# Performance work log

Measured on AMD Instinct MI355X. Metric: run time of the kernel, lower is better.

The kernel has to match this reference:

```python
import jax, jax.numpy as jnp
import numpy as np

T = 16          # timesteps
BATCH = 8       # video clips -> leading dim of x is BATCH*T = 128
C_IN = 768      # fixed by nn.Conv2d(768, redu_dim, 1)
D = 256         # redu_dim
K = 64          # num_centers
H = W = 28
EPS = 1e-12     # torch F.normalize eps


def _conv(x, w, padding):
    # x: [N,C,H,W], w: [O,I,kh,kw]
    return jax.lax.conv_general_dilated(
        x, w, window_strides=(1, 1), padding=padding,
        dimension_numbers=('NCHW', 'OIHW', 'NCHW'))


def setup_inputs() -> dict:
    key = jax.random.key(0)
    ks = jax.random.split(key, 9)
    x = jax.random.normal(ks[0], (BATCH * T, C_IN, H, W), dtype=jnp.float32)
    redu_w = jax.random.normal(ks[1], (D, C_IN, 1, 1), jnp.float32) * 0.02
    redu_b = jnp.zeros((D,), jnp.float32)
    share_w = jax.random.normal(ks[2], (K, D, 1, 1), jnp.float32) * 0.05
    share_b = jnp.zeros((K,), jnp.float32)
    U_z = jax.random.normal(ks[3], (K, K, 3, 3), jnp.float32) * 0.04
    U_r = jax.random.normal(ks[4], (K, K, 3, 3), jnp.float32) * 0.04
    U_h = jax.random.normal(ks[5], (K, K, 3, 3), jnp.float32) * 0.04
    centers = jax.random.normal(ks[6], (K, D), jnp.float32) * 0.06
    return {"x": x, "redu_w": redu_w, "redu_b": redu_b,
            "share_w": share_w, "share_b": share_b,
            "U_z": U_z, "U_r": U_r, "U_h": U_h,
            "centers": centers, "timesteps": T}


def reference(x, redu_w, redu_b, share_w, share_b, U_z, U_r, U_h, centers, timesteps):
    t = timesteps
    bt, _, h, w = x.shape
    b = bt // t
    k = share_w.shape[0]
    d = redu_w.shape[0]

    # channel reduction (1x1 conv)
    xr = _conv(x, redu_w, 'VALID') + redu_b[None, :, None, None]        # [bt,d,h,w]
    # shared assignment logits (1x1 conv)
    wxb = _conv(xr, share_w, 'VALID') + share_b[None, :, None, None]     # [bt,k,h,w]
    wxb = wxb.reshape(b, t, k, h, w).transpose(1, 0, 2, 3, 4)            # [t,b,k,h,w]

    # sequential ConvGRU over timesteps
    h0 = jnp.zeros((b, k, h, w), x.dtype)
    def step(h_tm1, w_t):
        z = jax.nn.sigmoid(w_t + _conv(h_tm1, U_z, 'SAME'))
        r = jax.nn.sigmoid(w_t + _conv(h_tm1, U_r, 'SAME'))
        hh = jnp.tanh(w_t + _conv(r * h_tm1, U_h, 'SAME'))
        h_new = (1.0 - z) * hh + z * h_tm1
        return h_new, h_new
    _, hs = jax.lax.scan(step, h0, wxb)                                  # [t,b,k,h,w]

    assign = hs.transpose(1, 0, 2, 3, 4).reshape(b * t, k, h * w)        # [bt,k,hw]
    # softmax over centers per spatial location
    assign = jax.nn.softmax(assign, axis=1)

    # VLAD aggregation
    a_sum = assign.sum(axis=-1, keepdims=True)                           # [bt,k,1]
    a = a_sum * centers[None]                                            # [bt,k,d]
    xf = xr.reshape(b * t, d, h * w)                                     # [bt,d,hw]
    vlad = jnp.einsum('bkp,bdp->bkd', assign, xf) - a                    # [bt,k,d]

    vlad = vlad.reshape(b, t, k, d).sum(axis=1)                          # [b,k,d]
    # intra-norm over feature dim, then global L2 norm
    vlad = vlad / jnp.maximum(jnp.linalg.norm(vlad, axis=2, keepdims=True), EPS)
    vlad = vlad.reshape(b, k * d)
    vlad = vlad / jnp.maximum(jnp.linalg.norm(vlad, axis=1, keepdims=True), EPS)
    return vlad
```

## Files before the change

kernel.cpp:

```cpp
#include <hip/hip_runtime.h>
#include <hip/hip_bf16.h>

#define T_ 16
#define B_ 8
#define CIN 768
#define D_ 256
#define K_ 64
#define HW 784
#define W_ 28

typedef short short8 __attribute__((ext_vector_type(8)));
typedef short short4v __attribute__((ext_vector_type(4)));
typedef float floatx4 __attribute__((ext_vector_type(4)));
typedef unsigned short ushort_t;

__device__ __forceinline__ unsigned short f2bf(float x) {
    union { float f; unsigned u; } v; v.f = x;
    unsigned u = v.u;
    unsigned r = (u + 0x7fffu + ((u >> 16) & 1u)) >> 16;
    return (unsigned short)r;
}
__device__ __forceinline__ float bf2f(unsigned short h) {
    union { unsigned u; float f; } v; v.u = ((unsigned)h) << 16; return v.f;
}

__device__ __forceinline__ float block_reduce_sum_256(float v) {
    for (int off = 32; off > 0; off >>= 1) v += __shfl_down(v, off, 64);
    __shared__ float red[4];
    __shared__ float tot;
    int lane = threadIdx.x & 63, wid = threadIdx.x >> 6;
    if (lane == 0) red[wid] = v;
    __syncthreads();
    if (threadIdx.x == 0) tot = red[0] + red[1] + red[2] + red[3];
    __syncthreads();
    return tot;
}

__global__ __launch_bounds__(256) void cvt_weights(
    const float* __restrict__ rw, const float* __restrict__ sw,
    const float* __restrict__ Uz, const float* __restrict__ Ur,
    const float* __restrict__ Uh,
    ushort_t* __restrict__ whi, ushort_t* __restrict__ wlo,
    ushort_t* __restrict__ shi, ushort_t* __restrict__ slo,
    ushort_t* __restrict__ azh, ushort_t* __restrict__ azl,
    ushort_t* __restrict__ ahh, ushort_t* __restrict__ ahl)
{
    int i = blockIdx.x * 256 + threadIdx.x;
    const int nR = D_ * CIN;
    const int nS = K_ * D_;
    const int nZR = 128 * 576;
    const int nH = 64 * 576;
    if (i < nR) {
        float x = rw[i];
        unsigned short h = f2bf(x);
        whi[i] = h; wlo[i] = f2bf(x - bf2f(h));
    } else if (i < nR + nS) {
        int j = i - nR;
        float x = sw[j];
        unsigned short h = f2bf(x);
        shi[j] = h; slo[j] = f2bf(x - bf2f(h));
    } else if (i < nR + nS + nZR) {
        int j = i - nR - nS;
        int row = j / 576, kk = j - row * 576;
        int tap = kk >> 6, c = kk & 63;
        const float* U = (row < 64) ? Uz : Ur;
        float x = U[(((size_t)(row & 63)) * 64 + c) * 9 + tap];
        unsigned short h = f2bf(x);
        azh[j] = h; azl[j] = f2bf(x - bf2f(h));
    } else if (i < nR + nS + nZR + nH) {
        int j = i - nR - nS - nZR;
        int row = j / 576, kk = j - row * 576;
        int tap = kk >> 6, c = kk & 63;
        float x = Uh[(((size_t)row) * 64 + c) * 9 + tap];
        unsigned short h = f2bf(x);
        ahh[j] = h; ahl[j] = f2bf(x - bf2f(h));
    }
}

template<int BM>
__global__ __launch_bounds__(256, 2) void mfma_conv1x1(
    const float* __restrict__ X, const ushort_t* __restrict__ Whi,
    const ushort_t* __restrict__ Wlo, const float* __restrict__ bias,
    float* __restrict__ Out, int Kdim)
{
    const int nt = blockIdx.x, bt = blockIdx.z;
    const int p0 = nt * 112;
    const int tid = threadIdx.x, lane = tid & 63, wv = tid >> 6;
    const float* Xb = X + (size_t)bt * Kdim * HW;
    float* Ob = Out + (size_t)bt * BM * HW;

    __shared__ ushort_t lA[2][BM * 40];
    __shared__ ushort_t lB[2][112 * 40];

    constexpr int NI = (BM == 256) ? 7 : 2;
    floatx4 acc[4][NI];
#pragma unroll
    for (int a = 0; a < 4; ++a)
#pragma unroll
        for (int b = 0; b < NI; ++b) acc[a][b] = (floatx4){0.f, 0.f, 0.f, 0.f};

    const int NKS = Kdim / 32;
    for (int ks = 0; ks < NKS; ++ks) {
        const int k0 = ks * 32;
#pragma unroll
        for (int i = 0; i < BM / 64; ++i) {
            int ch = tid + i * 256;
            int m = ch >> 2, j = ch & 3;
            uint4 hv = *(const uint4*)(Whi + (size_t)m * Kdim + k0 + j * 8);
            uint4 lv = *(const uint4*)(Wlo + (size_t)m * Kdim + k0 + j * 8);
            *(uint4*)&lA[0][m * 40 + j * 8] = hv;
            *(uint4*)&lA[1][m * 40 + j * 8] = lv;
        }
#pragma unroll
        for (int i = 0; i < 14; ++i) {
            int e = tid + i * 256;
            int cc = e / 112, pp = e - cc * 112;
            float xv = Xb[(size_t)(k0 + cc) * HW + p0 + pp];
            unsigned short h = f2bf(xv);
            lB[0][pp * 40 + cc] = h;
            lB[1][pp * 40 + cc] = f2bf(xv - bf2f(h));
        }
        __syncthreads();

        short8 ahi[4], alo[4];
        const int mbase = (BM == 256) ? wv * 64 : 0;
        const int koff = (lane >> 4) * 8;
#pragma unroll
        for (int mi = 0; mi < 4; ++mi) {
            int m = mbase + mi * 16 + (lane & 15);
            ahi[mi] = *(const short8*)&lA[0][m * 40 + koff];
            alo[mi] = *(const short8*)&lA[1][m * 40 + koff];
        }
        if constexpr (BM == 256) {
#pragma unroll
            for (int ni = 0; ni < 7; ++ni) {
                int n = ni * 16 + (lane & 15);
                short8 bhi = *(const short8*)&lB[0][n * 40 + koff];
                short8 blo = *(const short8*)&lB[1][n * 40 + koff];
#pragma unroll
                for (int mi = 0; mi < 4; ++mi) {
                    acc[mi][ni] = __builtin_amdgcn_mfma_f32_16x16x32_bf16(ahi[mi], bhi, acc[mi][ni], 0, 0, 0);
                    acc[mi][ni] = __builtin_amdgcn_mfma_f32_16x16x32_bf16(ahi[mi], blo, acc[mi][ni], 0, 0, 0);
                    acc[mi][ni] = __builtin_amdgcn_mfma_f32_16x16x32_bf16(alo[mi], bhi, acc[mi][ni], 0, 0, 0);
                }
            }
        } else {
#pragma unroll
            for (int nj = 0; nj < 2; ++nj) {
                int ni = wv * 2 + nj;
                if (ni >= 7) break;
                int n = ni * 16 + (lane & 15);
                short8 bhi = *(const short8*)&lB[0][n * 40 + koff];
                short8 blo = *(const short8*)&lB[1][n * 40 + koff];
#pragma unroll
                for (int mi = 0; mi < 4; ++mi) {
                    acc[mi][nj] = __builtin_amdgcn_mfma_f32_16x16x32_bf16(ahi[mi], bhi, acc[mi][nj], 0, 0, 0);
                    acc[mi][nj] = __builtin_amdgcn_mfma_f32_16x16x32_bf16(ahi[mi], blo, acc[mi][nj], 0, 0, 0);
                    acc[mi][nj] = __builtin_amdgcn_mfma_f32_16x16x32_bf16(alo[mi], bhi, acc[mi][nj], 0, 0, 0);
                }
            }
        }
        __syncthreads();
    }

    if constexpr (BM == 256) {
#pragma unroll
        for (int mi = 0; mi < 4; ++mi) {
            int m0g = wv * 64 + mi * 16 + ((lane >> 4) << 2);
#pragma unroll
            for (int ni = 0; ni < 7; ++ni) {
                int p = p0 + ni * 16 + (lane & 15);
#pragma unroll
                for (int r = 0; r < 4; ++r)
                    Ob[(size_t)(m0g + r) * HW + p] = acc[mi][ni][r] + bias[m0g + r];
            }
        }
    } else {
#pragma unroll
        for (int nj = 0; nj < 2; ++nj) {
            int ni = wv * 2 + nj;
            if (ni >= 7) break;
            int p = p0 + ni * 16 + (lane & 15);
#pragma unroll
            for (int mi = 0; mi < 4; ++mi) {
                int m0g = mi * 16 + ((lane >> 4) << 2);
#pragma unroll
                for (int r = 0; r < 4; ++r)
                    Ob[(size_t)(m0g + r) * HW + p] = acc[mi][nj][r] + bias[m0g + r];
            }
        }
    }
}

__device__ __forceinline__ void stage_tile(
    const ushort_t* __restrict__ ghi, const ushort_t* __restrict__ glo,
    ushort_t* Bhi, ushort_t* Blo, int y0, int tid)
{
    for (int e = tid; e < 6 * 30 * 8; e += 256) {
        int r = e / 240, rem = e - r * 240;
        int lx = rem >> 3, j = rem & 7;
        int gy = y0 - 1 + r, gx = lx - 1;
        short8 vh = {0, 0, 0, 0, 0, 0, 0, 0};
        short8 vl = {0, 0, 0, 0, 0, 0, 0, 0};
        if (gy >= 0 && gy < 28 && gx >= 0 && gx < 28) {
            size_t go = ((size_t)(gy * 28 + gx)) * 64 + j * 8;
            vh = *(const short8*)(ghi + go);
            vl = *(const short8*)(glo + go);
        }
        int lo = (r * 30 + lx) * 72 + j * 8;
        *(short8*)&Bhi[lo] = vh;
        *(short8*)&Blo[lo] = vl;
    }
}

__device__ __forceinline__ void gru_gemm(
    const ushort_t* __restrict__ Ahi, const ushort_t* __restrict__ Alo,
    int arow, int Astride,
    const ushort_t* Bhi, const ushort_t* Blo, int lane, floatx4 acc[7])
{
    const int koff8 = (lane >> 4) * 8;
    const int li = lane & 15;
    int yb[7], xb[7];
#pragma unroll
    for (int nf = 0; nf < 7; ++nf) {
        int pp = nf * 16 + li;
        yb[nf] = pp / 28; xb[nf] = pp - yb[nf] * 28;
    }
    for (int tap = 0; tap < 9; ++tap) {
        int dy = tap / 3, dx = tap - dy * 3;
#pragma unroll
        for (int ch = 0; ch < 2; ++ch) {
            int kk = tap * 64 + ch * 32 + koff8;
            short8 ahi = *(const short8*)(Ahi + (size_t)arow * Astride + kk);
            short8 alo = *(const short8*)(Alo + (size_t)arow * Astride + kk);
            int cbase = ch * 32 + koff8;
#pragma unroll
            for (int nf = 0; nf < 7; ++nf) {
                int o = ((yb[nf] + dy) * 30 + xb[nf] + dx) * 72 + cbase;
                short8 bhi = *(const short8*)&Bhi[o];
                short8 blo = *(const short8*)&Blo[o];
                acc[nf] = __builtin_amdgcn_mfma_f32_16x16x32_bf16(ahi, bhi, acc[nf], 0, 0, 0);
                acc[nf] = __builtin_amdgcn_mfma_f32_16x16x32_bf16(ahi, blo, acc[nf], 0, 0, 0);
                acc[nf] = __builtin_amdgcn_mfma_f32_16x16x32_bf16(alo, bhi, acc[nf], 0, 0, 0);
            }
        }
    }
}

__global__ __launch_bounds__(256, 2) void gru_zr_mfma(
    const ushort_t* __restrict__ hhi, const ushort_t* __restrict__ hlo,
    const ushort_t* __restrict__ azh, const ushort_t* __restrict__ azl,
    const float* __restrict__ wxb, const float* __restrict__ hprev_f,
    float* __restrict__ zbuf, ushort_t* __restrict__ rhi, ushort_t* __restrict__ rlo,
    int t)
{
    int rt = blockIdx.x, b = blockIdx.y, half = blockIdx.z;
    int y0 = rt * 4;
    int tid = threadIdx.x, lane = tid & 63, wv = tid >> 6;

    __shared__ ushort_t Bhi[6 * 30 * 72];
    __shared__ ushort_t Blo[6 * 30 * 72];
    stage_tile(hhi + (size_t)b * HW * 64, hlo + (size_t)b * HW * 64, Bhi, Blo, y0, tid);
    __syncthreads();

    floatx4 acc[7];
#pragma unroll
    for (int nf = 0; nf < 7; ++nf) acc[nf] = (floatx4){0.f, 0.f, 0.f, 0.f};

    int arow = half * 64 + wv * 16 + (lane & 15);
    gru_gemm(azh, azl, arow, 576, Bhi, Blo, lane, acc);

    int kbase = wv * 16 + ((lane >> 4) << 2);
    const float* wx = wxb + (((size_t)b * T_ + t) * K_) * HW;
    const float* hp = hprev_f + (size_t)b * K_ * HW;
#pragma unroll
    for (int nf = 0; nf < 7; ++nf) {
        int p = y0 * 28 + nf * 16 + (lane & 15);
        if (half == 0) {
#pragma unroll
            for (int r = 0; r < 4; ++r) {
                int k = kbase + r;
                float g = 1.f / (1.f + __expf(-(wx[(size_t)k * HW + p] + acc[nf][r])));
                zbuf[((size_t)b * K_ + k) * HW + p] = g;
            }
        } else {
            short4v vh, vl;
#pragma unroll
            for (int r = 0; r < 4; ++r) {
                int k = kbase + r;
                float g = 1.f / (1.f + __expf(-(wx[(size_t)k * HW + p] + acc[nf][r])));
                float rh = g * hp[(size_t)k * HW + p];
                unsigned short h = f2bf(rh);
                vh[r] = h; vl[r] = f2bf(rh - bf2f(h));
            }
            size_t o = (size_t)(b * HW + p) * 64 + kbase;
            *(short4v*)(rhi + o) = vh;
            *(short4v*)(rlo + o) = vl;
        }
    }
}

__global__ __launch_bounds__(256, 2) void gru_h_mfma(
    const ushort_t* __restrict__ rhi, const ushort_t* __restrict__ rlo,
    const ushort_t* __restrict__ ahh, const ushort_t* __restrict__ ahl,
    const float* __restrict__ wxb, const float* __restrict__ hprev_f,
    const float* __restrict__ zbuf, float* __restrict__ hs_t,
    ushort_t* __restrict__ hhi, ushort_t* __restrict__ hlo, int t)
{
    int rt = blockIdx.x, b = blockIdx.y;
    int y0 = rt * 4;
    int tid = threadIdx.x, lane = tid & 63, wv = tid >> 6;

    __shared__ ushort_t Bhi[6 * 30 * 72];
    __shared__ ushort_t Blo[6 * 30 * 72];
    stage_tile(rhi + (size_t)b * HW * 64, rlo + (size_t)b * HW * 64, Bhi, Blo, y0, tid);
    __syncthreads();

    floatx4 acc[7];
#pragma unroll
    for (int nf = 0; nf < 7; ++nf) acc[nf] = (floatx4){0.f, 0.f, 0.f, 0.f};

    int arow = wv * 16 + (lane & 15);
    gru_gemm(ahh, ahl, arow, 576, Bhi, Blo, lane, acc);

    int kbase = wv * 16 + ((lane >> 4) << 2);
    const float* wx = wxb + (((size_t)b * T_ + t) * K_) * HW;
    const float* hp = hprev_f + (size_t)b * K_ * HW;
#pragma unroll
    for (int nf = 0; nf < 7; ++nf) {
        int p = y0 * 28 + nf * 16 + (lane & 15);
        short4v vh, vl;
#pragma unroll
        for (int r = 0; r < 4; ++r) {
            int k = kbase + r;
            float xv = wx[(size_t)k * HW + p] + acc[nf][r];
            float e2 = __expf(2.f * xv);
            float th = 1.f - 2.f / (e2 + 1.f);
            float z = zbuf[((size_t)b * K_ + k) * HW + p];
            float hpv = hp[(size_t)k * HW + p];
            float hn = (1.f - z) * th + z * hpv;
            hs_t[((size_t)b * K_ + k) * HW + p] = hn;
            unsigned short h = f2bf(hn);
            vh[r] = h; vl[r] = f2bf(hn - bf2f(h));
        }
        size_t o = (size_t)(b * HW + p) * 64 + kbase;
        *(short4v*)(hhi + o) = vh;
        *(short4v*)(hlo + o) = vl;
    }
}

__global__ __launch_bounds__(256) void softmax_k(float* __restrict__ hs)
{
    int q = blockIdx.x;
    float* base = hs + (size_t)q * K_ * HW;
    for (int p = threadIdx.x; p < HW; p += 256) {
        float v[64];
        float m = -1e30f;
#pragma unroll
        for (int k = 0; k < 64; ++k) {
            v[k] = base[(size_t)k * HW + p];
            m = fmaxf(m, v[k]);
        }
        float s = 0.f;
#pragma unroll
        for (int k = 0; k < 64; ++k) {
            v[k] = __expf(v[k] - m);
            s += v[k];
        }
        float inv = 1.f / s;
#pragma unroll
        for (int k = 0; k < 64; ++k)
            base[(size_t)k * HW + p] = v[k] * inv;
    }
}

__global__ __launch_bounds__(256) void asum_k(const float* __restrict__ hs,
                                              float* __restrict__ asum)
{
    int bid = blockIdx.x; int b = bid >> 6, k = bid & 63;
    float s = 0.f;
    for (int t = 0; t < T_; ++t) {
        const float* row = hs + (((size_t)t * B_ + b) * K_ + k) * HW;
        for (int p = threadIdx.x; p < HW; p += 256) s += row[p];
    }
    float tot = block_reduce_sum_256(s);
    if (threadIdx.x == 0) asum[bid] = tot;
}

__global__ __launch_bounds__(256) void vlad_k(const float* __restrict__ assign,
    const float* __restrict__ xr, float* __restrict__ vladt)
{
    int dt = blockIdx.x, t = blockIdx.y, b = blockIdx.z;
    int q = t * B_ + b, bt = b * T_ + t, d0 = dt * 64;
    const float* ab = assign + (size_t)q * K_ * HW;
    const float* xb = xr + (size_t)bt * D_ * HW;
    __shared__ float As[16][68];
    __shared__ float Xs[16][68];
    int tx = threadIdx.x & 15, ty = threadIdx.x >> 4;
    float acc[4][4] = {{0.f}};

    for (int p0 = 0; p0 < HW; p0 += 16) {
#pragma unroll
        for (int it = 0; it < 4; ++it) {
            int e = threadIdx.x + it * 256;
            int row = e >> 4, pp = e & 15;
            As[pp][row] = ab[(size_t)row * HW + p0 + pp];
            Xs[pp][row] = xb[(size_t)(d0 + row) * HW + p0 + pp];
        }
        __syncthreads();
#pragma unroll
        for (int pp = 0; pp < 16; ++pp) {
            float4 a = *(const float4*)&As[pp][ty * 4];
            float4 xv = *(const float4*)&Xs[pp][tx * 4];
            float av[4] = {a.x, a.y, a.z, a.w};
            float xvv[4] = {xv.x, xv.y, xv.z, xv.w};
#pragma unroll
            for (int r = 0; r < 4; ++r)
#pragma unroll
                for (int s = 0; s < 4; ++s)
                    acc[r][s] = fmaf(av[r], xvv[s], acc[r][s]);
        }
        __syncthreads();
    }
#pragma unroll
    for (int r = 0; r < 4; ++r) {
        int k = ty * 4 + r;
        float4 o = {acc[r][0], acc[r][1], acc[r][2], acc[r][3]};
        *(float4*)&vladt[((size_t)bt * K_ + k) * D_ + d0 + tx * 4] = o;
    }
}

__global__ __launch_bounds__(256) void norm1_k(const float* __restrict__ vladt,
    const float* __restrict__ asum, const float* __restrict__ centers,
    float* __restrict__ out)
{
    int bid = blockIdx.x; int b = bid >> 6, k = bid & 63; int d = threadIdx.x;
    float acc = 0.f;
#pragma unroll
    for (int t = 0; t < T_; ++t)
        acc += vladt[(((size_t)b * T_ + t) * K_ + k) * D_ + d];
    acc -= asum[bid] * centers[(size_t)k * D_ + d];
    float ss = block_reduce_sum_256(acc * acc);
    float n = fmaxf(sqrtf(ss), 1e-12f);
    out[((size_t)b * K_ + k) * D_ + d] = acc / n;
}

__global__ __launch_bounds__(256) void norm2_k(float* __restrict__ out)
{
    int b = blockIdx.x;
    float* v = out + (size_t)b * (K_ * D_);
    float s = 0.f;
    for (int i = threadIdx.x; i < K_ * D_; i += 256) {
        float x = v[i];
        s = fmaf(x, x, s);
    }
    float tot = block_reduce_sum_256(s);
    float n = fmaxf(sqrtf(tot), 1e-12f);
    for (int i = threadIdx.x; i < K_ * D_; i += 256) v[i] = v[i] / n;
}

extern "C" void kernel_launch(void* const* d_in, const int* in_sizes, int n_in,
                              void* d_out, int out_size, void* d_ws, size_t ws_size,
                              hipStream_t stream)
{
    const float* x       = (const float*)d_in[0];
    const float* redu_w  = (const float*)d_in[1];
    const float* redu_b  = (const float*)d_in[2];
    const float* share_w = (const float*)d_in[3];
    const float* share_b = (const float*)d_in[4];
    const float* Uz      = (const float*)d_in[5];
    const float* Ur      = (const float*)d_in[6];
    const float* Uh      = (const float*)d_in[7];
    const float* centers = (const float*)d_in[8];

    float* ws = (float*)d_ws;
    const size_t SZ_XR   = (size_t)128 * D_ * HW;
    const size_t SZ_WXB  = (size_t)128 * K_ * HW;
    const size_t SZ_HS   = (size_t)T_ * B_ * K_ * HW;
    const size_t SZ_PLANE= (size_t)B_ * K_ * HW;

    float* xr    = ws;
    float* wxb   = xr + SZ_XR;
    float* hs    = wxb + SZ_WXB;
    float* h0    = hs + SZ_HS;
    float* zbuf  = h0 + SZ_PLANE;
    float* asumb = zbuf + SZ_PLANE;
    float* wsplit= asumb + 512;
    float* area  = wsplit + 323584;

    ushort_t* whi = (ushort_t*)wsplit;
    ushort_t* wlo = whi + 196608;
    ushort_t* shi = wlo + 196608;
    ushort_t* slo = shi + 16384;
    ushort_t* azh = slo + 16384;
    ushort_t* azl = azh + 73728;
    ushort_t* ahh = azl + 73728;
    ushort_t* ahl = ahh + 36864;

    float* vladt = area;
    ushort_t* hhi = (ushort_t*)area;
    ushort_t* hlo = hhi + SZ_PLANE;
    ushort_t* rhi = hlo + SZ_PLANE;
    ushort_t* rlo = rhi + SZ_PLANE;

    hipMemsetAsync(h0, 0, SZ_PLANE * sizeof(float), stream);
    hipMemsetAsync(hhi, 0, 2 * SZ_PLANE * sizeof(ushort_t), stream);

    cvt_weights<<<dim3((D_ * CIN + K_ * D_ + 128 * 576 + 64 * 576 + 255) / 256),
                  256, 0, stream>>>(redu_w, share_w, Uz, Ur, Uh,
                                    whi, wlo, shi, slo, azh, azl, ahh, ahl);

    mfma_conv1x1<256><<<dim3(7, 1, 128), 256, 0, stream>>>(x, whi, wlo, redu_b, xr, CIN);
    mfma_conv1x1<64><<<dim3(7, 1, 128), 256, 0, stream>>>(xr, shi, slo, share_b, wxb, D_);

    for (int t = 0; t < T_; ++t) {
        const float* hp = (t == 0) ? h0 : hs + (size_t)(t - 1) * SZ_PLANE;
        gru_zr_mfma<<<dim3(7, 8, 2), 256, 0, stream>>>(hhi, hlo, azh, azl, wxb, hp,
                                                       zbuf, rhi, rlo, t);
        gru_h_mfma<<<dim3(7, 8), 256, 0, stream>>>(rhi, rlo, ahh, ahl, wxb, hp, zbuf,
                                                   hs + (size_t)t * SZ_PLANE, hhi, hlo, t);
    }

    softmax_k<<<128, 256, 0, stream>>>(hs);
    asum_k<<<512, 256, 0, stream>>>(hs, asumb);

    vlad_k<<<dim3(4, 16, 8), 256, 0, stream>>>(hs, xr, vladt);
    norm1_k<<<512, 256, 0, stream>>>(vladt, asumb, centers, (float*)d_out);
    norm2_k<<<8, 256, 0, stream>>>((float*)d_out);
}
```

Before: 795.5 us.

## Split GRU conv tiles to one row per block and stream conv1x1 weights from global

The GRU z/r and h kernels now process one image row per block instead of four, launching four times as many blocks (224/448 instead of 56/112) with a smaller 3-row LDS halo and two MFMA fragments per wave. This spreads the small sequential per-timestep launches across more CUs. It also re-reads the halo rows more often and wastes four lanes in the second fragment. The 1x1 conv kernels drop the LDS staging of weights, loading A fragments directly from global, and vectorise the X staging into 8-channel short8 writes. They also raise launch-bound occupancy hints.

```diff
diff --git a/kernel.cpp b/kernel.cpp
--- a/kernel.cpp
+++ b/kernel.cpp
@@ -77,8 +77,8 @@
     }
 }
 
-template<int BM>
-__global__ __launch_bounds__(256, 2) void mfma_conv1x1(
+template<int BM, int MINW>
+__global__ __launch_bounds__(256, MINW) void mfma_conv1x1(
     const float* __restrict__ X, const ushort_t* __restrict__ Whi,
     const ushort_t* __restrict__ Wlo, const float* __restrict__ bias,
     float* __restrict__ Out, int Kdim)
@@ -89,7 +89,6 @@
     const float* Xb = X + (size_t)bt * Kdim * HW;
     float* Ob = Out + (size_t)bt * BM * HW;
 
-    __shared__ ushort_t lA[2][BM * 40];
     __shared__ ushort_t lB[2][112 * 40];
 
     constexpr int NI = (BM == 256) ? 7 : 2;
@@ -98,38 +97,36 @@
     for (int a = 0; a < 4; ++a)
 #pragma unroll
         for (int b = 0; b < NI; ++b) acc[a][b] = (floatx4){0.f, 0.f, 0.f, 0.f};
+
+    const int koff = (lane >> 4) * 8;
+    const int mbase = (BM == 256) ? wv * 64 : 0;
 
     const int NKS = Kdim / 32;
     for (int ks = 0; ks < NKS; ++ks) {
         const int k0 = ks * 32;
 #pragma unroll
-        for (int i = 0; i < BM / 64; ++i) {
-            int ch = tid + i * 256;
-            int m = ch >> 2, j = ch & 3;
-            uint4 hv = *(const uint4*)(Whi + (size_t)m * Kdim + k0 + j * 8);
-            uint4 lv = *(const uint4*)(Wlo + (size_t)m * Kdim + k0 + j * 8);
-            *(uint4*)&lA[0][m * 40 + j * 8] = hv;
-            *(uint4*)&lA[1][m * 40 + j * 8] = lv;
-        }
-#pragma unroll
-        for (int i = 0; i < 14; ++i) {
-            int e = tid + i * 256;
-            int cc = e / 112, pp = e - cc * 112;
-            float xv = Xb[(size_t)(k0 + cc) * HW + p0 + pp];
-            unsigned short h = f2bf(xv);
-            lB[0][pp * 40 + cc] = h;
-            lB[1][pp * 40 + cc] = f2bf(xv - bf2f(h));
+        for (int u = tid; u < 448; u += 256) {
+            int j = u / 112, pp = u - j * 112;
+            const float* xp = Xb + (size_t)(k0 + j * 8) * HW + p0 + pp;
+            short8 vh, vl;
+#pragma unroll
+            for (int c = 0; c < 8; ++c) {
+                float xv = xp[(size_t)c * HW];
+                unsigned short h = f2bf(xv);
+                vh[c] = (short)h;
+                vl[c] = (short)f2bf(xv - bf2f(h));
+            }
+            *(short8*)&lB[0][pp * 40 + j * 8] = vh;
+            *(short8*)&lB[1][pp * 40 + j * 8] = vl;
         }
         __syncthreads();
 
         short8 ahi[4], alo[4];
-        const int mbase = (BM == 256) ? wv * 64 : 0;
-        const int koff = (lane >> 4) * 8;
 #pragma unroll
         for (int mi = 0; mi < 4; ++mi) {
             int m = mbase + mi * 16 + (lane & 15);
-            ahi[mi] = *(const short8*)&lA[0][m * 40 + koff];
-            alo[mi] = *(const short8*)&lA[1][m * 40 + koff];
+            ahi[mi] = *(const short8*)(Whi + (size_t)m * Kdim + k0 + koff);
+            alo[mi] = *(const short8*)(Wlo + (size_t)m * Kdim + k0 + koff);
         }
         if constexpr (BM == 256) {
 #pragma unroll
@@ -192,11 +189,11 @@
     }
 }
 
-__device__ __forceinline__ void stage_tile(
+__device__ __forceinline__ void stage_tile3(
     const ushort_t* __restrict__ ghi, const ushort_t* __restrict__ glo,
     ushort_t* Bhi, ushort_t* Blo, int y0, int tid)
 {
-    for (int e = tid; e < 6 * 30 * 8; e += 256) {
+    for (int e = tid; e < 3 * 30 * 8; e += 256) {
         int r = e / 240, rem = e - r * 240;
         int lx = rem >> 3, j = rem & 7;
         int gy = y0 - 1 + r, gx = lx - 1;
@@ -213,69 +210,70 @@
     }
 }
 
-__device__ __forceinline__ void gru_gemm(
-    const ushort_t* __restrict__ Ahi, const ushort_t* __restrict__ Alo,
-    int arow, int Astride,
-    const ushort_t* Bhi, const ushort_t* Blo, int lane, floatx4 acc[7])
+__device__ __forceinline__ void gru_gemm1(
+    const ushort_t* __restrict__ Ahi, const ushort_t* __restrict__ Alo, int arow,
+    const ushort_t* Bhi, const ushort_t* Blo, int lane, floatx4 acc[2])
 {
     const int koff8 = (lane >> 4) * 8;
     const int li = lane & 15;
-    int yb[7], xb[7];
-#pragma unroll
-    for (int nf = 0; nf < 7; ++nf) {
-        int pp = nf * 16 + li;
-        yb[nf] = pp / 28; xb[nf] = pp - yb[nf] * 28;
-    }
+    const int xb0 = li;
+    const int xb1 = (li < 12) ? 16 + li : 0;
+#pragma unroll
     for (int tap = 0; tap < 9; ++tap) {
-        int dy = tap / 3, dx = tap - dy * 3;
+        const int dy = tap / 3, dx = tap - dy * 3;
 #pragma unroll
         for (int ch = 0; ch < 2; ++ch) {
             int kk = tap * 64 + ch * 32 + koff8;
-            short8 ahi = *(const short8*)(Ahi + (size_t)arow * Astride + kk);
-            short8 alo = *(const short8*)(Alo + (size_t)arow * Astride + kk);
+            short8 ahi = *(const short8*)(Ahi + (size_t)arow * 576 + kk);
+            short8 alo = *(const short8*)(Alo + (size_t)arow * 576 + kk);
             int cbase = ch * 32 + koff8;
-#pragma unroll
-            for (int nf = 0; nf < 7; ++nf) {
-                int o = ((yb[nf] + dy) * 30 + xb[nf] + dx) * 72 + cbase;
-                short8 bhi = *(const short8*)&Bhi[o];
-                short8 blo = *(const short8*)&Blo[o];
-                acc[nf] = __builtin_amdgcn_mfma_f32_16x16x32_bf16(ahi, bhi, acc[nf], 0, 0, 0);
-                acc[nf] = __builtin_amdgcn_mfma_f32_16x16x32_bf16(ahi, blo, acc[nf], 0, 0, 0);
-                acc[nf] = __builtin_amdgcn_mfma_f32_16x16x32_bf16(alo, bhi, acc[nf], 0, 0, 0);
-            }
-        }
-    }
-}
-
-__global__ __launch_bounds__(256, 2) void gru_zr_mfma(
+            int o0 = (dy * 30 + xb0 + dx) * 72 + cbase;
+            int o1 = (dy * 30 + xb1 + dx) * 72 + cbase;
+            short8 bhi0 = *(const short8*)&Bhi[o0];
+            short8 blo0 = *(const short8*)&Blo[o0];
+            short8 bhi1 = *(const short8*)&Bhi[o1];
+            short8 blo1 = *(const short8*)&Blo[o1];
+            acc[0] = __builtin_amdgcn_mfma_f32_16x16x32_bf16(ahi, bhi0, acc[0], 0, 0, 0);
+            acc[0] = __builtin_amdgcn_mfma_f32_16x16x32_bf16(ahi, blo0, acc[0], 0, 0, 0);
+            acc[0] = __builtin_amdgcn_mfma_f32_16x16x32_bf16(alo, bhi0, acc[0], 0, 0, 0);
+            acc[1] = __builtin_amdgcn_mfma_f32_16x16x32_bf16(ahi, bhi1, acc[1], 0, 0, 0);
+            acc[1] = __builtin_amdgcn_mfma_f32_16x16x32_bf16(ahi, blo1, acc[1], 0, 0, 0);
+            acc[1] = __builtin_amdgcn_mfma_f32_16x16x32_bf16(alo, bhi1, acc[1], 0, 0, 0);
+        }
+    }
+}
+
+__global__ __launch_bounds__(256, 4) void gru_zr_mfma(
     const ushort_t* __restrict__ hhi, const ushort_t* __restrict__ hlo,
     const ushort_t* __restrict__ azh, const ushort_t* __restrict__ azl,
     const float* __restrict__ wxb, const float* __restrict__ hprev_f,
     float* __restrict__ zbuf, ushort_t* __restrict__ rhi, ushort_t* __restrict__ rlo,
     int t)
 {
-    int rt = blockIdx.x, b = blockIdx.y, half = blockIdx.z;
-    int y0 = rt * 4;
+    int y0 = blockIdx.x, b = blockIdx.y, half = blockIdx.z;
     int tid = threadIdx.x, lane = tid & 63, wv = tid >> 6;
 
-    __shared__ ushort_t Bhi[6 * 30 * 72];
-    __shared__ ushort_t Blo[6 * 30 * 72];
-    stage_tile(hhi + (size_t)b * HW * 64, hlo + (size_t)b * HW * 64, Bhi, Blo, y0, tid);
+    __shared__ ushort_t Bhi[3 * 30 * 72];
+    __shared__ ushort_t Blo[3 * 30 * 72];
+    stage_tile3(hhi + (size_t)b * HW * 64, hlo + (size_t)b * HW * 64, Bhi, Blo, y0, tid);
     __syncthreads();
 
-    floatx4 acc[7];
-#pragma unroll
-    for (int nf = 0; nf < 7; ++nf) acc[nf] = (floatx4){0.f, 0.f, 0.f, 0.f};
+    floatx4 acc[2];
+    acc[0] = (floatx4){0.f, 0.f, 0.f, 0.f};
+    acc[1] = (floatx4){0.f, 0.f, 0.f, 0.f};
 
     int arow = half * 64 + wv * 16 + (lane & 15);
-    gru_gemm(azh, azl, arow, 576, Bhi, Blo, lane, acc);
-
+    gru_gemm1(azh, azl, arow, Bhi, Blo, lane, acc);
+
+    int li = lane & 15;
     int kbase = wv * 16 + ((lane >> 4) << 2);
     const float* wx = wxb + (((size_t)b * T_ + t) * K_) * HW;
     const float* hp = hprev_f + (size_t)b * K_ * HW;
 #pragma unroll
-    for (int nf = 0; nf < 7; ++nf) {
-        int p = y0 * 28 + nf * 16 + (lane & 15);
+    for (int nf = 0; nf < 2; ++nf) {
+        int pp = nf * 16 + li;
+        if (pp >= 28) break;
+        int p = y0 * 28 + pp;
         if (half == 0) {
 #pragma unroll
             for (int r = 0; r < 4; ++r) {
@@ -300,35 +298,37 @@
     }
 }
 
-__global__ __launch_bounds__(256, 2) void gru_h_mfma(
+__global__ __launch_bounds__(256, 4) void gru_h_mfma(
     const ushort_t* __restrict__ rhi, const ushort_t* __restrict__ rlo,
     const ushort_t* __restrict__ ahh, const ushort_t* __restrict__ ahl,
     const float* __restrict__ wxb, const float* __restrict__ hprev_f,
     const float* __restrict__ zbuf, float* __restrict__ hs_t,
     ushort_t* __restrict__ hhi, ushort_t* __restrict__ hlo, int t)
 {
-    int rt = blockIdx.x, b = blockIdx.y;
-    int y0 = rt * 4;
+    int y0 = blockIdx.x, b = blockIdx.y;
     int tid = threadIdx.x, lane = tid & 63, wv = tid >> 6;
 
-    __shared__ ushort_t Bhi[6 * 30 * 72];
-    __shared__ ushort_t Blo[6 * 30 * 72];
-    stage_tile(rhi + (size_t)b * HW * 64, rlo + (size_t)b * HW * 64, Bhi, Blo, y0, tid);
+    __shared__ ushort_t Bhi[3 * 30 * 72];
+    __shared__ ushort_t Blo[3 * 30 * 72];
+    stage_tile3(rhi + (size_t)b * HW * 64, rlo + (size_t)b * HW * 64, Bhi, Blo, y0, tid);
     __syncthreads();
 
-    floatx4 acc[7];
-#pragma unroll
-    for (int nf = 0; nf < 7; ++nf) acc[nf] = (floatx4){0.f, 0.f, 0.f, 0.f};
+    floatx4 acc[2];
+    acc[0] = (floatx4){0.f, 0.f, 0.f, 0.f};
+    acc[1] = (floatx4){0.f, 0.f, 0.f, 0.f};
 
     int arow = wv * 16 + (lane & 15);
-    gru_gemm(ahh, ahl, arow, 576, Bhi, Blo, lane, acc);
-
+    gru_gemm1(ahh, ahl, arow, Bhi, Blo, lane, acc);
+
+    int li = lane & 15;
     int kbase = wv * 16 + ((lane >> 4) << 2);
     const float* wx = wxb + (((size_t)b * T_ + t) * K_) * HW;
     const float* hp = hprev_f + (size_t)b * K_ * HW;
 #pragma unroll
-    for (int nf = 0; nf < 7; ++nf) {
-        int p = y0 * 28 + nf * 16 + (lane & 15);
+    for (int nf = 0; nf < 2; ++nf) {
+        int pp = nf * 16 + li;
+        if (pp >= 28) break;
+        int p = y0 * 28 + pp;
         short4v vh, vl;
 #pragma unroll
         for (int r = 0; r < 4; ++r) {
@@ -510,15 +510,15 @@
                   256, 0, stream>>>(redu_w, share_w, Uz, Ur, Uh,
                                     whi, wlo, shi, slo, azh, azl, ahh, ahl);
 
-    mfma_conv1x1<256><<<dim3(7, 1, 128), 256, 0, stream>>>(x, whi, wlo, redu_b, xr, CIN);
-    mfma_conv1x1<64><<<dim3(7, 1, 128), 256, 0, stream>>>(xr, shi, slo, share_b, wxb, D_);
+    mfma_conv1x1<256, 3><<<dim3(7, 1, 128), 256, 0, stream>>>(x, whi, wlo, redu_b, xr, CIN);
+    mfma_conv1x1<64, 4><<<dim3(7, 1, 128), 256, 0, stream>>>(xr, shi, slo, share_b, wxb, D_);
 
     for (int t = 0; t < T_; ++t) {
         const float* hp = (t == 0) ? h0 : hs + (size_t)(t - 1) * SZ_PLANE;
-        gru_zr_mfma<<<dim3(7, 8, 2), 256, 0, stream>>>(hhi, hlo, azh, azl, wxb, hp,
-                                                       zbuf, rhi, rlo, t);
-        gru_h_mfma<<<dim3(7, 8), 256, 0, stream>>>(rhi, rlo, ahh, ahl, wxb, hp, zbuf,
-                                                   hs + (size_t)t * SZ_PLANE, hhi, hlo, t);
+        gru_zr_mfma<<<dim3(28, 8, 2), 256, 0, stream>>>(hhi, hlo, azh, azl, wxb, hp,
+                                                        zbuf, rhi, rlo, t);
+        gru_h_mfma<<<dim3(28, 8), 256, 0, stream>>>(rhi, rlo, ahh, ahl, wxb, hp, zbuf,
+                                                    hs + (size_t)t * SZ_PLANE, hhi, hlo, t);
     }
 
     softmax_k<<<128, 256, 0, stream>>>(hs);
```

Result: no change. 791.7 us (-0.5%).
